# Kernel tuning notes

Hardware: AMD Instinct MI355X
Metric: run time of the kernel (lower is better)

Reference implementation:

```python
import jax, jax.numpy as jnp
import numpy as np

N_NODES = 50000
N_EDGES = 800000
IN_DIM, HID_DIM, OUT_DIM, N_HEADS = 256, 256, 64, 4
ATT_DIM = OUT_DIM * 2 + 1  # 129


def setup_inputs() -> dict:
    key = jax.random.key(0)
    ks = jax.random.split(key, 8)
    s = 0.05
    return {
        "x": jax.random.normal(ks[0], (N_NODES, IN_DIM), dtype=jnp.float32),
        "idx": jax.random.randint(ks[1], (2, N_EDGES), 0, N_NODES, dtype=jnp.int32),
        "elem": jax.random.uniform(ks[2], (N_EDGES,), dtype=jnp.float32),
        "W1": jax.random.normal(ks[3], (N_HEADS, IN_DIM, HID_DIM), dtype=jnp.float32) * s,
        "b1": jnp.zeros((N_HEADS, HID_DIM), jnp.float32),
        "W2": jax.random.normal(ks[4], (N_HEADS, HID_DIM, OUT_DIM), dtype=jnp.float32) * s,
        "b2": jnp.zeros((N_HEADS, OUT_DIM), jnp.float32),
        "A1": jax.random.normal(ks[5], (N_HEADS, ATT_DIM, ATT_DIM), dtype=jnp.float32) * s,
        "ab1": jnp.zeros((N_HEADS, ATT_DIM), jnp.float32),
        "A2": jax.random.normal(ks[6], (N_HEADS, ATT_DIM, 1), dtype=jnp.float32) * s,
        "ab2": jnp.zeros((N_HEADS, 1), jnp.float32),
    }


def reference(x, idx, elem, W1, b1, W2, b2, A1, ab1, A2, ab2):
    row, col = idx[0], idx[1]
    n = x.shape[0]

    def head(w1, bb1, w2, bb2, a1, aab1, a2, aab2):
        # 2-layer node MLP: [N, in] -> [N, out]
        feats = jnp.maximum(x @ w1 + bb1, 0.0) @ w2 + bb2
        # gather edge endpoints + edge value -> [E, 2*out+1]
        x_cat = jnp.concatenate([feats[row], feats[col], elem[:, None]], axis=1)
        # 2-layer edge attention MLP -> scalar per edge
        hid = jnp.maximum(x_cat @ a1 + aab1, 0.0)
        e1 = (hid @ a2 + aab2)[:, 0]
        e1 = jax.nn.leaky_relu(e1, negative_slope=0.2)
        w = jnp.exp(e1 - jnp.max(e1))  # global-max-stabilized exp
        # spmm: scatter weighted neighbor features into rows
        pooled = jax.ops.segment_sum(w[:, None] * feats[col], row, num_segments=n)
        row_sum = jax.ops.segment_sum(w, row, num_segments=n) + 1e-10
        return pooled / row_sum[:, None]  # [N, out]

    h = jax.vmap(head)(W1, b1, W2, b2, A1, ab1, A2, ab2)  # [H, N, out]
    return jnp.transpose(h, (1, 0, 2)).reshape(n, -1)  # concat heads -> [N, H*out]
```

## Files before the change

### kernel.cpp

```cpp
#include <hip/hip_runtime.h>
#include <hip/hip_bf16.h>

#define NNODES 50000
#define NEDGES 800000
#define IN_DIM 256
#define HID_DIM 256
#define OUT_DIM 64
#define NHEADS 4
#define ATT_DIM 129
#define PDIM 128
#define PJROWS 144
#define MAXD 64

#define XS_LD 264
#define FS_LD 72

#define LOG2E 1.44269504088896340736f

typedef unsigned short u16;
typedef unsigned char u8;
typedef __attribute__((ext_vector_type(8))) short bf16x8;
typedef __attribute__((ext_vector_type(4))) float f32x4;
typedef __attribute__((ext_vector_type(2))) float f32x2;
typedef __attribute__((ext_vector_type(2))) _Float16 h16x2;
typedef __fp16 hh2 __attribute__((ext_vector_type(2)));

__device__ __forceinline__ u16 f2bf(float f) {
  union { __hip_bfloat16 b; u16 u; } v;
  v.b = __float2bfloat16(f);
  return v.u;
}
__device__ __forceinline__ float bf2f(u16 b) {
  return __uint_as_float(((unsigned int)b) << 16);
}
__device__ __forceinline__ h16x2 u2h2(unsigned int u) {
  union { unsigned int u; h16x2 h; } v; v.u = u; return v.h;
}
__device__ __forceinline__ unsigned int h2u(h16x2 h) {
  union { h16x2 h; unsigned int u; } v; v.h = h; return v.u;
}
__device__ __forceinline__ h16x2 pkrtz(float a, float b) {
  return __builtin_bit_cast(h16x2, __builtin_amdgcn_cvt_pkrtz(a, b));
}
__device__ __forceinline__ unsigned int cvt_pk_bf16(float a, float b) {
  unsigned int r;
  asm("v_cvt_pk_bf16_f32 %0, %1, %2" : "=v"(r) : "v"(a), "v"(b));
  return r;
}

__device__ __forceinline__ float dpp_sum16(float x) {
  int v;
  v = __builtin_amdgcn_update_dpp(0, __float_as_int(x), 0xB1, 0xF, 0xF, true);
  x += __int_as_float(v);
  v = __builtin_amdgcn_update_dpp(0, __float_as_int(x), 0x4E, 0xF, 0xF, true);
  x += __int_as_float(v);
  v = __builtin_amdgcn_update_dpp(0, __float_as_int(x), 0x141, 0xF, 0xF, true);
  x += __int_as_float(v);
  v = __builtin_amdgcn_update_dpp(0, __float_as_int(x), 0x140, 0xF, 0xF, true);
  x += __int_as_float(v);
  return x;
}

__global__ __launch_bounds__(256) void prep_kernel(
    const float* __restrict__ x, const float* __restrict__ W1,
    const float* __restrict__ W2, const float* __restrict__ A1,
    const float* __restrict__ ab1, const float* __restrict__ A2,
    const float* __restrict__ ab2, u16* __restrict__ xb,
    u16* __restrict__ W1T, u16* __restrict__ W2T,
    u16* __restrict__ A1Tr, u16* __restrict__ A1Tc,
    uint4* __restrict__ thE, uint4* __restrict__ thA2, uint4* __restrict__ thB1,
    float4* __restrict__ th_tail, unsigned int* __restrict__ cnt)
{
  int id = blockIdx.x * 256 + threadIdx.x;
  {
    float4 a = *(const float4*)(x + (size_t)id * 8);
    float4 b = *(const float4*)(x + (size_t)id * 8 + 4);
    ushort4 o0, o1;
    o0.x = f2bf(a.x); o0.y = f2bf(a.y); o0.z = f2bf(a.z); o0.w = f2bf(a.w);
    o1.x = f2bf(b.x); o1.y = f2bf(b.y); o1.z = f2bf(b.z); o1.w = f2bf(b.w);
    *(ushort4*)(xb + (size_t)id * 8) = o0;
    *(ushort4*)(xb + (size_t)id * 8 + 4) = o1;
  }
  if (id < NHEADS * 256 * 256) {
    int h = id >> 16, j = (id >> 8) & 255, k = id & 255;
    W1T[id] = f2bf(W1[(size_t)h * 65536 + k * 256 + j]);
  }
  if (id < NHEADS * 64 * 256) {
    int h = id >> 14, d = (id >> 8) & 63, j = id & 255;
    W2T[id] = f2bf(W2[(size_t)h * 16384 + j * 64 + d]);
  }
  if (id < NHEADS * PJROWS * 64) {
    int h = id / (PJROWS * 64);
    int rem = id % (PJROWS * 64);
    int j = rem >> 6, d = rem & 63;
    A1Tr[id] = (j < ATT_DIM) ? f2bf(A1[(size_t)h * 16641 + d * ATT_DIM + j]) : (u16)0;
    A1Tc[id] = (j < ATT_DIM) ? f2bf(A1[(size_t)h * 16641 + (64 + d) * ATT_DIM + j]) : (u16)0;
  }
  if (id < NHEADS * 16) {
    int h = id >> 4, m = id & 15;
    const float* Erow = A1 + (size_t)h * 16641 + (size_t)128 * ATT_DIM;
    uint4 e, a, b;
    unsigned int* ep = (unsigned int*)&e;
    unsigned int* ap = (unsigned int*)&a;
    unsigned int* bp = (unsigned int*)&b;
#pragma unroll
    for (int p = 0; p < 4; ++p) {
      int j = m * 8 + 2 * p;
      ep[p] = h2u(pkrtz(Erow[j], Erow[j + 1]));
      ap[p] = h2u(pkrtz(A2[h * ATT_DIM + j] * LOG2E, A2[h * ATT_DIM + j + 1] * LOG2E));
      bp[p] = h2u(pkrtz(ab1[h * ATT_DIM + j], ab1[h * ATT_DIM + j + 1]));
    }
    thE[id] = e; thA2[id] = a; thB1[id] = b;
  }
  if (id < NHEADS) {
    const float* Erow = A1 + (size_t)id * 16641 + (size_t)128 * ATT_DIM;
    th_tail[id] = make_float4(Erow[128], ab1[id * ATT_DIM + 128],
                              A2[id * ATT_DIM + 128] * LOG2E, ab2[id] * LOG2E);
  }
  if (id < NNODES) cnt[id] = 0;
}

__global__ __launch_bounds__(256) void fill_kernel(const int* __restrict__ idx,
                                                   const float* __restrict__ elem,
                                                   unsigned int* __restrict__ cnt,
                                                   int2* __restrict__ ce)
{
  int e = blockIdx.x * 256 + threadIdx.x;
  if (e < NEDGES) {
    int r = idx[e];
    unsigned int p = atomicAdd(&cnt[r], 1u);
    if (p < MAXD) {
      int2 v;
      v.x = idx[NEDGES + e] << 10;
      v.y = __float_as_int(elem[e]);
      ce[r * MAXD + p] = v;
    }
  }
}

__global__ __launch_bounds__(256) void mlp_mfma_kernel(
    const u16* __restrict__ xb, const u16* __restrict__ W1T,
    const float* __restrict__ b1, const u16* __restrict__ W2T,
    const float* __restrict__ b2, const u16* __restrict__ A1Tr,
    const u16* __restrict__ A1Tc, u8* __restrict__ PF,
    u16* __restrict__ Pr, u16* __restrict__ Prt, u16* __restrict__ Pct)
{
  __shared__ u16 xs[64 * XS_LD];
  __shared__ u16 hs[64 * XS_LD];
  const int h = blockIdx.y;
  const int n0 = blockIdx.x * 64;
  const int t = threadIdx.x;
  const int wv = t >> 6;
  const int l = t & 63;
  const int lr = l & 15;
  const int lq = l >> 4;

#pragma unroll
  for (int q = 0; q < 8; ++q) {
    int fi = q * 256 + t;
    int row = fi >> 5, c8 = fi & 31;
    int n = n0 + row;
    uint4 v = make_uint4(0, 0, 0, 0);
    if (n < NNODES) v = *(const uint4*)(xb + (size_t)n * IN_DIM + c8 * 8);
    *(uint4*)&xs[row * XS_LD + c8 * 8] = v;
  }
  __syncthreads();

  f32x4 acc[4][4];
#pragma unroll
  for (int ji = 0; ji < 4; ++ji)
#pragma unroll
    for (int ni = 0; ni < 4; ++ni) acc[ji][ni] = f32x4{0.f, 0.f, 0.f, 0.f};

  const u16* W1b = W1T + ((size_t)h * 256 + wv * 64) * 256;
#pragma unroll
  for (int kk = 0; kk < 8; ++kk) {
    const int ko = kk * 32 + lq * 8;
    bf16x8 w[4], xv[4];
#pragma unroll
    for (int ji = 0; ji < 4; ++ji)
      w[ji] = *(const bf16x8*)(W1b + (size_t)(ji * 16 + lr) * 256 + ko);
#pragma unroll
    for (int ni = 0; ni < 4; ++ni)
      xv[ni] = *(const bf16x8*)&xs[(ni * 16 + lr) * XS_LD + ko];
#pragma unroll
    for (int ji = 0; ji < 4; ++ji)
#pragma unroll
      for (int ni = 0; ni < 4; ++ni)
        acc[ji][ni] = __builtin_amdgcn_mfma_f32_16x16x32_bf16(w[ji], xv[ni], acc[ji][ni], 0, 0, 0);
  }
#pragma unroll
  for (int ji = 0; ji < 4; ++ji) {
    float4 bv = *(const float4*)(b1 + h * HID_DIM + wv * 64 + ji * 16 + lq * 4);
#pragma unroll
    for (int ni = 0; ni < 4; ++ni) {
      f32x4 v = acc[ji][ni];
      unsigned lo = cvt_pk_bf16(fmaxf(v[0] + bv.x, 0.f), fmaxf(v[1] + bv.y, 0.f));
      unsigned hi = cvt_pk_bf16(fmaxf(v[2] + bv.z, 0.f), fmaxf(v[3] + bv.w, 0.f));
      *(uint2*)&hs[(ni * 16 + lr) * XS_LD + wv * 64 + ji * 16 + lq * 4] = make_uint2(lo, hi);
    }
  }
  __syncthreads();

  f32x4 acc2[4];
#pragma unroll
  for (int ni = 0; ni < 4; ++ni) acc2[ni] = f32x4{0.f, 0.f, 0.f, 0.f};
  const u16* W2b = W2T + ((size_t)h * 64 + wv * 16) * 256;
#pragma unroll
  for (int kk = 0; kk < 8; ++kk) {
    const int ko = kk * 32 + lq * 8;
    bf16x8 wd = *(const bf16x8*)(W2b + (size_t)lr * 256 + ko);
#pragma unroll
    for (int ni = 0; ni < 4; ++ni) {
      bf16x8 hv = *(const bf16x8*)&hs[(ni * 16 + lr) * XS_LD + ko];
      acc2[ni] = __builtin_amdgcn_mfma_f32_16x16x32_bf16(wd, hv, acc2[ni], 0, 0, 0);
    }
  }
  u16* fs = xs;
  {
    float4 bv = *(const float4*)(b2 + h * OUT_DIM + wv * 16 + lq * 4);
    const int d0 = wv * 16 + lq * 4;
#pragma unroll
    for (int ni = 0; ni < 4; ++ni) {
      f32x4 v = acc2[ni];
      unsigned lo = cvt_pk_bf16(v[0] + bv.x, v[1] + bv.y);
      unsigned hi = cvt_pk_bf16(v[2] + bv.z, v[3] + bv.w);
      *(uint2*)&fs[(ni * 16 + lr) * FS_LD + d0] = make_uint2(lo, hi);
      int n = n0 + ni * 16 + lr;
      if (n < NNODES)
        *(uint2*)(PF + (size_t)n * 1024 + h * 256 + 128 + d0 * 2) = make_uint2(lo, hi);
    }
  }
  __syncthreads();

  for (int c = wv; c < 18; c += 4) {
    const int rc = c / 9;
    const int nf = c % 9;
    const u16* Ab = (rc ? A1Tc : A1Tr) + ((size_t)h * PJROWS + nf * 16) * 64;
    f32x4 acc3[4];
#pragma unroll
    for (int ni = 0; ni < 4; ++ni) acc3[ni] = f32x4{0.f, 0.f, 0.f, 0.f};
#pragma unroll
    for (int kk = 0; kk < 2; ++kk) {
      const int ko = kk * 32 + lq * 8;
      bf16x8 aj = *(const bf16x8*)(Ab + (size_t)lr * 64 + ko);
#pragma unroll
      for (int ni = 0; ni < 4; ++ni) {
        bf16x8 fv = *(const bf16x8*)&fs[(ni * 16 + lr) * FS_LD + ko];
        acc3[ni] = __builtin_amdgcn_mfma_f32_16x16x32_bf16(aj, fv, acc3[ni], 0, 0, 0);
      }
    }
#pragma unroll
    for (int ni = 0; ni < 4; ++ni) {
      int n = n0 + ni * 16 + lr;
      if (n >= NNODES) continue;
      if (nf == 8) {
        if (lq == 0) {
          u16 vb = f2bf(acc3[ni][0]);
          if (rc == 0) Prt[(size_t)h * NNODES + n] = vb;
          else         Pct[(size_t)n * NHEADS + h] = vb;
        }
      } else {
        const int j0 = nf * 16 + lq * 4;
        f32x4 v = acc3[ni];
        if (rc == 0) {
          unsigned lo = cvt_pk_bf16(v[0], v[1]);
          unsigned hi = cvt_pk_bf16(v[2], v[3]);
          *(uint2*)&Pr[((size_t)h * NNODES + n) * PDIM + j0] = make_uint2(lo, hi);
        } else {
          unsigned pk = __builtin_amdgcn_cvt_pk_fp8_f32(v[0], v[1], 0, false);
          pk = __builtin_amdgcn_cvt_pk_fp8_f32(v[2], v[3], pk, true);
          *(unsigned*)(PF + (size_t)n * 1024 + h * 256 + j0) = pk;
        }
      }
    }
  }
}

__global__ __launch_bounds__(256) void edge_csr_kernel(
    const u8* __restrict__ PF, const u16* __restrict__ Pr,
    const u16* __restrict__ Prt, const u16* __restrict__ Pct,
    const unsigned int* __restrict__ cnt, const int2* __restrict__ ce,
    const uint4* __restrict__ thE, const uint4* __restrict__ thA2,
    const uint4* __restrict__ thB1, const float4* __restrict__ th_tail,
    float* __restrict__ out)
{
  const int r = blockIdx.x;
  const int h = threadIdx.x >> 6;
  const int l = threadIdx.x & 63;
  const int g = l >> 4;
  const int m = l & 15;

  h16x2 Ej2[4], a2v2[4], prb2[4];
  {
    uint4 Eu = thE[h * 16 + m], Au = thA2[h * 16 + m], Bu = thB1[h * 16 + m];
    uint4 pru = *(const uint4*)(Pr + ((size_t)h * NNODES + r) * PDIM + m * 8);
    const unsigned int* pw = (const unsigned int*)&pru;
    const unsigned int* ep = (const unsigned int*)&Eu;
    const unsigned int* ap = (const unsigned int*)&Au;
    const unsigned int* bp = (const unsigned int*)&Bu;
#pragma unroll
    for (int p = 0; p < 4; ++p) {
      Ej2[p]  = u2h2(ep[p]);
      a2v2[p] = u2h2(ap[p]);
      float lo = __uint_as_float(pw[p] << 16);
      float hi = __uint_as_float(pw[p] & 0xffff0000u);
      prb2[p] = pkrtz(lo, hi) + u2h2(bp[p]);
    }
  }
  const float4 tl = th_tail[h];
  float Et = 0.f, prtb = 0.f, a2t = 0.f;
  if (m == 0) {
    Et = tl.x;
    prtb = bf2f(Prt[(size_t)h * NNODES + r]) + tl.y;
    a2t = tl.z;
  }
  const float ab2v = tl.w;
  const h16x2 zero2 = {(_Float16)0.f, (_Float16)0.f};

  const int deg = min((int)cnt[r], MAXD);
  const int2* cebase = ce + r * MAXD;

  float acc0 = 0.f, acc1 = 0.f, acc2a = 0.f, acc3a = 0.f, wsum = 0.f;

  for (int k0 = 0; k0 < deg; k0 += 4) {
    const int e0 = k0 + g;
    int2 c2 = cebase[(e0 < deg) ? e0 : (deg - 1)];
    const u8* p8 = PF + (unsigned)c2.x + h * 256;
    const float el = __int_as_float(c2.y);

    uint2 pc = *(const uint2*)(p8 + m * 8);
    ushort4 f4 = *(const ushort4*)(p8 + 128 + m * 8);
    float pctv = (m == 0) ? bf2f(Pct[((unsigned)c2.x >> 8) + h]) : 0.f;

    float tsum = fmaxf(fmaf(el, Et, prtb + pctv), 0.f) * a2t;

    f32x2 v01 = __builtin_amdgcn_cvt_pk_f32_fp8((int)pc.x, false);
    f32x2 v23 = __builtin_amdgcn_cvt_pk_f32_fp8((int)pc.x, true);
    f32x2 v45 = __builtin_amdgcn_cvt_pk_f32_fp8((int)pc.y, false);
    f32x2 v67 = __builtin_amdgcn_cvt_pk_f32_fp8((int)pc.y, true);
    h16x2 pch[4] = {pkrtz(v01[0], v01[1]), pkrtz(v23[0], v23[1]),
                    pkrtz(v45[0], v45[1]), pkrtz(v67[0], v67[1])};
    const h16x2 el2 = pkrtz(el, el);

#pragma unroll
    for (int p = 0; p < 4; ++p) {
      h16x2 s = prb2[p] + pch[p];
      s = __builtin_elementwise_fma(el2, Ej2[p], s);
      s = __builtin_elementwise_max(s, zero2);
      tsum = __builtin_amdgcn_fdot2(__builtin_bit_cast(hh2, s),
                                    __builtin_bit_cast(hh2, a2v2[p]), tsum, false);
    }

    tsum = dpp_sum16(tsum);

    float e1 = tsum + ab2v;
    e1 = fmaxf(e1, 0.2f * e1);
    float w = exp2f(e1);
    w = (e0 < deg) ? w : 0.f;

    acc0  = fmaf(w, bf2f(f4.x), acc0);
    acc1  = fmaf(w, bf2f(f4.y), acc1);
    acc2a = fmaf(w, bf2f(f4.z), acc2a);
    acc3a = fmaf(w, bf2f(f4.w), acc3a);
    wsum += w;
  }

#pragma unroll
  for (int sh = 16; sh <= 32; sh <<= 1) {
    acc0  += __shfl_xor(acc0, sh);
    acc1  += __shfl_xor(acc1, sh);
    acc2a += __shfl_xor(acc2a, sh);
    acc3a += __shfl_xor(acc3a, sh);
    wsum  += __shfl_xor(wsum, sh);
  }
  if (g == 0) {
    float inv = 1.0f / (wsum + 1e-10f);
    float4 o = make_float4(acc0 * inv, acc1 * inv, acc2a * inv, acc3a * inv);
    *(float4*)(out + (size_t)r * (NHEADS * OUT_DIM) + h * OUT_DIM + m * 4) = o;
  }
}

extern "C" void kernel_launch(void* const* d_in, const int* in_sizes, int n_in,
                              void* d_out, int out_size, void* d_ws, size_t ws_size,
                              hipStream_t stream) {
  const float* x    = (const float*)d_in[0];
  const int*   idx  = (const int*)d_in[1];
  const float* elem = (const float*)d_in[2];
  const float* W1   = (const float*)d_in[3];
  const float* b1   = (const float*)d_in[4];
  const float* W2   = (const float*)d_in[5];
  const float* b2   = (const float*)d_in[6];
  const float* A1   = (const float*)d_in[7];
  const float* ab1  = (const float*)d_in[8];
  const float* A2   = (const float*)d_in[9];
  const float* ab2  = (const float*)d_in[10];
  float* out = (float*)d_out;

  u16* xb  = (u16*)d_ws;
  int2* ce = (int2*)d_ws;
  u16* Pr  = xb + (size_t)NNODES * IN_DIM;
  u8*  PF  = (u8*)(Pr + (size_t)NHEADS * NNODES * PDIM);
  u16* Prt = (u16*)(PF + (size_t)NNODES * 1024);
  u16* Pct = Prt + (size_t)NHEADS * NNODES;
  unsigned int* cnt = (unsigned int*)(Pct + (size_t)NHEADS * NNODES);
  u16* W1T  = (u16*)(cnt + NNODES);
  u16* W2T  = W1T + NHEADS * 256 * 256;
  u16* A1Tr = W2T + NHEADS * 64 * 256;
  u16* A1Tc = A1Tr + NHEADS * PJROWS * 64;
  uint4* thE  = (uint4*)(A1Tc + NHEADS * PJROWS * 64);
  uint4* thA2 = thE + NHEADS * 16;
  uint4* thB1 = thA2 + NHEADS * 16;
  float4* th_tail = (float4*)(thB1 + NHEADS * 16);

  prep_kernel<<<NNODES * IN_DIM / 8 / 256, 256, 0, stream>>>(
      x, W1, W2, A1, ab1, A2, ab2, xb, W1T, W2T, A1Tr, A1Tc,
      thE, thA2, thB1, th_tail, cnt);

  dim3 gridM((NNODES + 63) / 64, NHEADS);
  mlp_mfma_kernel<<<gridM, 256, 0, stream>>>(xb, W1T, b1, W2T, b2, A1Tr, A1Tc,
                                             PF, Pr, Prt, Pct);

  fill_kernel<<<(NEDGES + 255) / 256, 256, 0, stream>>>(idx, elem, cnt, ce);

  edge_csr_kernel<<<NNODES, 256, 0, stream>>>(PF, Pr, Prt, Pct, cnt, ce,
                                              thE, thA2, thB1, th_tail, out);
}
```

Baseline: 343.1 us.

## Fuse CSR fill into prep, pack edges, store row projections in fp8, prefetch edges

```diff
diff --git a/kernel.cpp b/kernel.cpp
--- a/kernel.cpp
+++ b/kernel.cpp
@@ -19,6 +19,7 @@
 
 typedef unsigned short u16;
 typedef unsigned char u8;
+typedef unsigned int u32;
 typedef __attribute__((ext_vector_type(8))) short bf16x8;
 typedef __attribute__((ext_vector_type(4))) float f32x4;
 typedef __attribute__((ext_vector_type(2))) float f32x2;
@@ -31,19 +32,19 @@
   return v.u;
 }
 __device__ __forceinline__ float bf2f(u16 b) {
-  return __uint_as_float(((unsigned int)b) << 16);
-}
-__device__ __forceinline__ h16x2 u2h2(unsigned int u) {
-  union { unsigned int u; h16x2 h; } v; v.u = u; return v.h;
-}
-__device__ __forceinline__ unsigned int h2u(h16x2 h) {
-  union { h16x2 h; unsigned int u; } v; v.h = h; return v.u;
+  return __uint_as_float(((u32)b) << 16);
+}
+__device__ __forceinline__ h16x2 u2h2(u32 u) {
+  union { u32 u; h16x2 h; } v; v.u = u; return v.h;
+}
+__device__ __forceinline__ u32 h2u(h16x2 h) {
+  union { h16x2 h; u32 u; } v; v.h = h; return v.u;
 }
 __device__ __forceinline__ h16x2 pkrtz(float a, float b) {
   return __builtin_bit_cast(h16x2, __builtin_amdgcn_cvt_pkrtz(a, b));
 }
-__device__ __forceinline__ unsigned int cvt_pk_bf16(float a, float b) {
-  unsigned int r;
+__device__ __forceinline__ u32 cvt_pk_bf16(float a, float b) {
+  u32 r;
   asm("v_cvt_pk_bf16_f32 %0, %1, %2" : "=v"(r) : "v"(a), "v"(b));
   return r;
 }
@@ -62,14 +63,15 @@
 }
 
 __global__ __launch_bounds__(256) void prep_kernel(
-    const float* __restrict__ x, const float* __restrict__ W1,
+    const float* __restrict__ x, const int* __restrict__ idx,
+    const float* __restrict__ elem, const float* __restrict__ W1,
     const float* __restrict__ W2, const float* __restrict__ A1,
     const float* __restrict__ ab1, const float* __restrict__ A2,
     const float* __restrict__ ab2, u16* __restrict__ xb,
     u16* __restrict__ W1T, u16* __restrict__ W2T,
     u16* __restrict__ A1Tr, u16* __restrict__ A1Tc,
     uint4* __restrict__ thE, uint4* __restrict__ thA2, uint4* __restrict__ thB1,
-    float4* __restrict__ th_tail, unsigned int* __restrict__ cnt)
+    float4* __restrict__ th_tail, u32* __restrict__ cnt, u32* __restrict__ ce)
 {
   int id = blockIdx.x * 256 + threadIdx.x;
   {
@@ -81,6 +83,12 @@
     *(ushort4*)(xb + (size_t)id * 8) = o0;
     *(ushort4*)(xb + (size_t)id * 8 + 4) = o1;
   }
+  if (id < NEDGES) {
+    int r = idx[id];
+    u32 p = atomicAdd(&cnt[r], 1u);
+    if (p < MAXD)
+      ce[r * MAXD + p] = ((u32)f2bf(elem[id]) << 16) | (u32)idx[NEDGES + id];
+  }
   if (id < NHEADS * 256 * 256) {
     int h = id >> 16, j = (id >> 8) & 255, k = id & 255;
     W1T[id] = f2bf(W1[(size_t)h * 65536 + k * 256 + j]);
@@ -100,9 +108,7 @@
     int h = id >> 4, m = id & 15;
     const float* Erow = A1 + (size_t)h * 16641 + (size_t)128 * ATT_DIM;
     uint4 e, a, b;
-    unsigned int* ep = (unsigned int*)&e;
-    unsigned int* ap = (unsigned int*)&a;
-    unsigned int* bp = (unsigned int*)&b;
+    u32* ep = (u32*)&e; u32* ap = (u32*)&a; u32* bp = (u32*)&b;
 #pragma unroll
     for (int p = 0; p < 4; ++p) {
       int j = m * 8 + 2 * p;
@@ -117,25 +123,6 @@
     th_tail[id] = make_float4(Erow[128], ab1[id * ATT_DIM + 128],
                               A2[id * ATT_DIM + 128] * LOG2E, ab2[id] * LOG2E);
   }
-  if (id < NNODES) cnt[id] = 0;
-}
-
-__global__ __launch_bounds__(256) void fill_kernel(const int* __restrict__ idx,
-                                                   const float* __restrict__ elem,
-                                                   unsigned int* __restrict__ cnt,
-                                                   int2* __restrict__ ce)
-{
-  int e = blockIdx.x * 256 + threadIdx.x;
-  if (e < NEDGES) {
-    int r = idx[e];
-    unsigned int p = atomicAdd(&cnt[r], 1u);
-    if (p < MAXD) {
-      int2 v;
-      v.x = idx[NEDGES + e] << 10;
-      v.y = __float_as_int(elem[e]);
-      ce[r * MAXD + p] = v;
-    }
-  }
 }
 
 __global__ __launch_bounds__(256) void mlp_mfma_kernel(
@@ -143,7 +130,7 @@
     const float* __restrict__ b1, const u16* __restrict__ W2T,
     const float* __restrict__ b2, const u16* __restrict__ A1Tr,
     const u16* __restrict__ A1Tc, u8* __restrict__ PF,
-    u16* __restrict__ Pr, u16* __restrict__ Prt, u16* __restrict__ Pct)
+    u8* __restrict__ Pr8, u16* __restrict__ Prt, u16* __restrict__ Pct)
 {
   __shared__ u16 xs[64 * XS_LD];
   __shared__ u16 hs[64 * XS_LD];
@@ -195,8 +182,8 @@
 #pragma unroll
     for (int ni = 0; ni < 4; ++ni) {
       f32x4 v = acc[ji][ni];
-      unsigned lo = cvt_pk_bf16(fmaxf(v[0] + bv.x, 0.f), fmaxf(v[1] + bv.y, 0.f));
-      unsigned hi = cvt_pk_bf16(fmaxf(v[2] + bv.z, 0.f), fmaxf(v[3] + bv.w, 0.f));
+      u32 lo = cvt_pk_bf16(fmaxf(v[0] + bv.x, 0.f), fmaxf(v[1] + bv.y, 0.f));
+      u32 hi = cvt_pk_bf16(fmaxf(v[2] + bv.z, 0.f), fmaxf(v[3] + bv.w, 0.f));
       *(uint2*)&hs[(ni * 16 + lr) * XS_LD + wv * 64 + ji * 16 + lq * 4] = make_uint2(lo, hi);
     }
   }
@@ -223,8 +210,8 @@
 #pragma unroll
     for (int ni = 0; ni < 4; ++ni) {
       f32x4 v = acc2[ni];
-      unsigned lo = cvt_pk_bf16(v[0] + bv.x, v[1] + bv.y);
-      unsigned hi = cvt_pk_bf16(v[2] + bv.z, v[3] + bv.w);
+      u32 lo = cvt_pk_bf16(v[0] + bv.x, v[1] + bv.y);
+      u32 hi = cvt_pk_bf16(v[2] + bv.z, v[3] + bv.w);
       *(uint2*)&fs[(ni * 16 + lr) * FS_LD + d0] = make_uint2(lo, hi);
       int n = n0 + ni * 16 + lr;
       if (n < NNODES)
@@ -263,24 +250,19 @@
       } else {
         const int j0 = nf * 16 + lq * 4;
         f32x4 v = acc3[ni];
-        if (rc == 0) {
-          unsigned lo = cvt_pk_bf16(v[0], v[1]);
-          unsigned hi = cvt_pk_bf16(v[2], v[3]);
-          *(uint2*)&Pr[((size_t)h * NNODES + n) * PDIM + j0] = make_uint2(lo, hi);
-        } else {
-          unsigned pk = __builtin_amdgcn_cvt_pk_fp8_f32(v[0], v[1], 0, false);
-          pk = __builtin_amdgcn_cvt_pk_fp8_f32(v[2], v[3], pk, true);
-          *(unsigned*)(PF + (size_t)n * 1024 + h * 256 + j0) = pk;
-        }
+        u32 pk = __builtin_amdgcn_cvt_pk_fp8_f32(v[0], v[1], 0, false);
+        pk = __builtin_amdgcn_cvt_pk_fp8_f32(v[2], v[3], pk, true);
+        if (rc == 0) *(u32*)(Pr8 + ((size_t)h * NNODES + n) * PDIM + j0) = pk;
+        else         *(u32*)(PF + (size_t)n * 1024 + h * 256 + j0) = pk;
       }
     }
   }
 }
 
 __global__ __launch_bounds__(256) void edge_csr_kernel(
-    const u8* __restrict__ PF, const u16* __restrict__ Pr,
+    const u8* __restrict__ PF, const u8* __restrict__ Pr8,
     const u16* __restrict__ Prt, const u16* __restrict__ Pct,
-    const unsigned int* __restrict__ cnt, const int2* __restrict__ ce,
+    const u32* __restrict__ cnt, const u32* __restrict__ ce,
     const uint4* __restrict__ thE, const uint4* __restrict__ thA2,
     const uint4* __restrict__ thB1, const float4* __restrict__ th_tail,
     float* __restrict__ out)
@@ -291,21 +273,32 @@
   const int g = l >> 4;
   const int m = l & 15;
 
+  const int deg = min((int)cnt[r], MAXD);
+  if (deg == 0) {
+    if (g == 0)
+      *(float4*)(out + (size_t)r * (NHEADS * OUT_DIM) + h * OUT_DIM + m * 4) =
+          make_float4(0.f, 0.f, 0.f, 0.f);
+    return;
+  }
+
   h16x2 Ej2[4], a2v2[4], prb2[4];
   {
     uint4 Eu = thE[h * 16 + m], Au = thA2[h * 16 + m], Bu = thB1[h * 16 + m];
-    uint4 pru = *(const uint4*)(Pr + ((size_t)h * NNODES + r) * PDIM + m * 8);
-    const unsigned int* pw = (const unsigned int*)&pru;
-    const unsigned int* ep = (const unsigned int*)&Eu;
-    const unsigned int* ap = (const unsigned int*)&Au;
-    const unsigned int* bp = (const unsigned int*)&Bu;
+    uint2 pr8v = *(const uint2*)(Pr8 + ((size_t)h * NNODES + r) * PDIM + m * 8);
+    const u32* ep = (const u32*)&Eu;
+    const u32* ap = (const u32*)&Au;
+    const u32* bp = (const u32*)&Bu;
+    f32x2 q01 = __builtin_amdgcn_cvt_pk_f32_fp8((int)pr8v.x, false);
+    f32x2 q23 = __builtin_amdgcn_cvt_pk_f32_fp8((int)pr8v.x, true);
+    f32x2 q45 = __builtin_amdgcn_cvt_pk_f32_fp8((int)pr8v.y, false);
+    f32x2 q67 = __builtin_amdgcn_cvt_pk_f32_fp8((int)pr8v.y, true);
+    h16x2 prh[4] = {pkrtz(q01[0], q01[1]), pkrtz(q23[0], q23[1]),
+                    pkrtz(q45[0], q45[1]), pkrtz(q67[0], q67[1])};
 #pragma unroll
     for (int p = 0; p < 4; ++p) {
       Ej2[p]  = u2h2(ep[p]);
       a2v2[p] = u2h2(ap[p]);
-      float lo = __uint_as_float(pw[p] << 16);
-      float hi = __uint_as_float(pw[p] & 0xffff0000u);
-      prb2[p] = pkrtz(lo, hi) + u2h2(bp[p]);
+      prb2[p] = prh[p] + u2h2(bp[p]);
     }
   }
   const float4 tl = th_tail[h];
@@ -317,21 +310,27 @@
   }
   const float ab2v = tl.w;
   const h16x2 zero2 = {(_Float16)0.f, (_Float16)0.f};
-
-  const int deg = min((int)cnt[r], MAXD);
-  const int2* cebase = ce + r * MAXD;
+  const u8* PFh = PF + h * 256;
+
+  const u32* cebase = ce + r * MAXD;
 
   float acc0 = 0.f, acc1 = 0.f, acc2a = 0.f, acc3a = 0.f, wsum = 0.f;
 
+  u32 cv = cebase[min(g, deg - 1)];
+  u32 coloff = (cv & 0xffffu) << 10;
+  float el = __uint_as_float(cv & 0xffff0000u);
+  uint2 pc = *(const uint2*)(PFh + coloff + m * 8);
+  ushort4 f4 = *(const ushort4*)(PFh + coloff + 128 + m * 8);
+  float pctv = (m == 0) ? bf2f(Pct[(coloff >> 8) + h]) : 0.f;
+
   for (int k0 = 0; k0 < deg; k0 += 4) {
-    const int e0 = k0 + g;
-    int2 c2 = cebase[(e0 < deg) ? e0 : (deg - 1)];
-    const u8* p8 = PF + (unsigned)c2.x + h * 256;
-    const float el = __int_as_float(c2.y);
-
-    uint2 pc = *(const uint2*)(p8 + m * 8);
-    ushort4 f4 = *(const ushort4*)(p8 + 128 + m * 8);
-    float pctv = (m == 0) ? bf2f(Pct[((unsigned)c2.x >> 8) + h]) : 0.f;
+    int e1 = k0 + 4 + g;
+    u32 cvn = cebase[min(e1, deg - 1)];
+    u32 coln = (cvn & 0xffffu) << 10;
+    float eln = __uint_as_float(cvn & 0xffff0000u);
+    uint2 pcn = *(const uint2*)(PFh + coln + m * 8);
+    ushort4 f4n = *(const ushort4*)(PFh + coln + 128 + m * 8);
+    float pctvn = (m == 0) ? bf2f(Pct[(coln >> 8) + h]) : 0.f;
 
     float tsum = fmaxf(fmaf(el, Et, prtb + pctv), 0.f) * a2t;
 
@@ -354,16 +353,18 @@
 
     tsum = dpp_sum16(tsum);
 
-    float e1 = tsum + ab2v;
-    e1 = fmaxf(e1, 0.2f * e1);
-    float w = exp2f(e1);
-    w = (e0 < deg) ? w : 0.f;
+    float e1f = tsum + ab2v;
+    e1f = fmaxf(e1f, 0.2f * e1f);
+    float w = exp2f(e1f);
+    w = (k0 + g < deg) ? w : 0.f;
 
     acc0  = fmaf(w, bf2f(f4.x), acc0);
     acc1  = fmaf(w, bf2f(f4.y), acc1);
     acc2a = fmaf(w, bf2f(f4.z), acc2a);
     acc3a = fmaf(w, bf2f(f4.w), acc3a);
     wsum += w;
+
+    pc = pcn; f4 = f4n; el = eln; pctv = pctvn;
   }
 
 #pragma unroll
@@ -398,13 +399,13 @@
   float* out = (float*)d_out;
 
   u16* xb  = (u16*)d_ws;
-  int2* ce = (int2*)d_ws;
-  u16* Pr  = xb + (size_t)NNODES * IN_DIM;
-  u8*  PF  = (u8*)(Pr + (size_t)NHEADS * NNODES * PDIM);
+  u8*  Pr8 = (u8*)(xb + (size_t)NNODES * IN_DIM);
+  u8*  PF  = Pr8 + (size_t)NHEADS * NNODES * PDIM;
   u16* Prt = (u16*)(PF + (size_t)NNODES * 1024);
   u16* Pct = Prt + (size_t)NHEADS * NNODES;
-  unsigned int* cnt = (unsigned int*)(Pct + (size_t)NHEADS * NNODES);
-  u16* W1T  = (u16*)(cnt + NNODES);
+  u32* cnt = (u32*)(Pct + (size_t)NHEADS * NNODES);
+  u32* ce  = cnt + NNODES;
+  u16* W1T  = (u16*)(ce + (size_t)NNODES * MAXD);
   u16* W2T  = W1T + NHEADS * 256 * 256;
   u16* A1Tr = W2T + NHEADS * 64 * 256;
   u16* A1Tc = A1Tr + NHEADS * PJROWS * 64;
@@ -413,16 +414,16 @@
   uint4* thB1 = thA2 + NHEADS * 16;
   float4* th_tail = (float4*)(thB1 + NHEADS * 16);
 
+  (void)hipMemsetAsync(cnt, 0, (size_t)NNODES * sizeof(u32), stream);
+
   prep_kernel<<<NNODES * IN_DIM / 8 / 256, 256, 0, stream>>>(
-      x, W1, W2, A1, ab1, A2, ab2, xb, W1T, W2T, A1Tr, A1Tc,
-      thE, thA2, thB1, th_tail, cnt);
+      x, idx, elem, W1, W2, A1, ab1, A2, ab2, xb, W1T, W2T, A1Tr, A1Tc,
+      thE, thA2, thB1, th_tail, cnt, ce);
 
   dim3 gridM((NNODES + 63) / 64, NHEADS);
   mlp_mfma_kernel<<<gridM, 256, 0, stream>>>(xb, W1T, b1, W2T, b2, A1Tr, A1Tc,
-                                             PF, Pr, Prt, Pct);
-
-  fill_kernel<<<(NEDGES + 255) / 256, 256, 0, stream>>>(idx, elem, cnt, ce);
-
-  edge_csr_kernel<<<NNODES, 256, 0, stream>>>(PF, Pr, Prt, Pct, cnt, ce,
+                                             PF, Pr8, Prt, Pct);
+
+  edge_csr_kernel<<<NNODES, 256, 0, stream>>>(PF, Pr8, Prt, Pct, cnt, ce,
                                               thE, thA2, thB1, th_tail, out);
 }
```

New measurement: 349.2 us. No clear change (+1.8%).
